# Optimization experiments

Measured on AMD Instinct MI355X. Metric: run time of the kernel, lower is better.

The kernel has to match this reference:

```python
import jax, jax.numpy as jnp
import numpy as np

N, D, G, C, M = 4096, 256, 4, 10, 5  # nodes, feat dim, batches, centroids, clusterings


def setup_inputs() -> dict:
    key = jax.random.key(0)
    k1, k2, k3, k4 = jax.random.split(key, 4)
    adj = jax.random.uniform(k1, (N, N), dtype=jnp.float32)
    enc_rep = jax.random.normal(k2, (N, D), dtype=jnp.float32)
    batch_id = jax.random.randint(k3, (N,), 0, G, dtype=jnp.int32)
    cluster_labels = jax.random.randint(k4, (M, N), 0, C, dtype=jnp.int32)
    return {"adj": adj, "enc_rep": enc_rep, "batch_id": batch_id,
            "cluster_labels": cluster_labels, "top_k": 20, "top_k_inter": 10}


def reference(adj, enc_rep, batch_id, cluster_labels, top_k, top_k_inter):
    n = enc_rep.shape[0]
    NEG = jnp.float32(-1e30)
    rows = jnp.arange(n)

    # 'similarity' metric: raw inner-product similarity, full N x N once
    sim = enc_rep @ enc_rep.T                                # [N, N]
    same = batch_id[:, None] == batch_id[None, :]            # same-batch mask

    # intra: top_k+1 within own batch group, drop first (self) column
    intra_sim = jnp.where(same, sim, NEG)
    _, intra_idx = jax.lax.top_k(intra_sim, top_k + 1)
    intra_idx = intra_idx[:, 1:]                              # [N, top_k]

    # inter: top_k_inter among all other batch groups
    inter_sim = jnp.where(same, NEG, sim)
    _, inter_idx = jax.lax.top_k(inter_sim, top_k_inter)      # [N, top_k_inter]

    knn_idx = jnp.concatenate([intra_idx, inter_idx], axis=1)  # [N, k_tot]

    # rep_adj[j, i] = 1 iff j is a knn of i  (coo rows=neighbors, cols=node)
    B = jnp.zeros((n, n), jnp.float32).at[knn_idx, rows[:, None]].set(1.0)
    # common_adj = rep_adj * (rep_adj.T > 0), diag zeroed (mutual-knn graph)
    common = B * B.T
    common = common.at[rows, rows].set(0.0)

    # locality = knn_neighbor * adj
    locality = common * adj

    # padded-neighbor validity mask (I_knn_padded != -1 analog): mutual neighbors
    mutual = common[rows[:, None], knn_idx] > 0               # [N, k_tot]

    # per-clustering close-neighbor test, combined across clusterings
    nb_lbl = cluster_labels[:, knn_idx]                       # [M, N, k_tot]
    eq = cluster_labels[:, :, None] == nb_lbl                 # [M, N, k_tot]
    curr = eq | mutual[None]                                  # curr_close_nei = eq | bool_mask
    all_close = jnp.all(curr, axis=0)                         # AND across clusterings

    return locality, all_close.astype(jnp.float32)
```

## Files before the change

kernel.cpp:

```cpp
#include <hip/hip_runtime.h>
#include <hip/hip_bf16.h>
#include <cfloat>

#define NN 4096
#define DD 256
#define MM 5
#define K_TOT 30
#define TGT_INTRA 32
#define TGT_INTER 24
#define CAND_CAP 64

typedef __attribute__((ext_vector_type(8))) short bf16x8;
typedef __attribute__((ext_vector_type(4))) float f32x4;

__device__ __forceinline__ void async16(const void* g, void* l) {
    __builtin_amdgcn_global_load_lds((__attribute__((address_space(1))) void*)g,
                                     (__attribute__((address_space(3))) void*)l,
                                     16, 0, 0);
}

__global__ __launch_bounds__(256) void convert_bf16(const float* __restrict__ E,
                                                    ushort* __restrict__ Eb) {
    const int idx = blockIdx.x * 256 + threadIdx.x;
    const float4 f = ((const float4*)E)[idx];
    ushort4 h;
    {
        __hip_bfloat16 a = __float2bfloat16(f.x); h.x = *(ushort*)&a;
        __hip_bfloat16 b = __float2bfloat16(f.y); h.y = *(ushort*)&b;
        __hip_bfloat16 c = __float2bfloat16(f.z); h.z = *(ushort*)&c;
        __hip_bfloat16 d = __float2bfloat16(f.w); h.w = *(ushort*)&d;
    }
    ((ushort4*)Eb)[idx] = h;
}

__global__ __launch_bounds__(256) void gemm_bf16(const ushort* __restrict__ Eb,
                                                 ushort* __restrict__ simb) {
    __shared__ union {
        struct { ushort A[128 * 32]; ushort B[128 * 32]; } s;
        ushort stage[128 * 136];
    } lds;

    const int t = threadIdx.x;
    const int w = t >> 6, lane = t & 63;
    const int quad = lane >> 4, mr = lane & 15;
    const int rowBase = blockIdx.y * 128, colBase = blockIdx.x * 128;
    const int waveRow = (w & 1) * 64, waveCol = (w >> 1) * 64;

    const int lrow = lane >> 2;
    const int lslot = lane & 3;
    const int gchunk = lslot ^ ((lrow >> 1) & 3);

    f32x4 acc[4][4];
#pragma unroll
    for (int a = 0; a < 4; ++a)
#pragma unroll
        for (int b = 0; b < 4; ++b) acc[a][b] = (f32x4)(0.0f);

    for (int kc = 0; kc < DD; kc += 32) {
#pragma unroll
        for (int n = 0; n < 2; ++n) {
            const int r = w * 32 + n * 16 + lrow;
            const ushort* ga = Eb + (size_t)(rowBase + r) * DD + kc + gchunk * 8;
            const ushort* gb = Eb + (size_t)(colBase + r) * DD + kc + gchunk * 8;
            async16(ga, &lds.s.A[(w * 32 + n * 16) * 32]);
            async16(gb, &lds.s.B[(w * 32 + n * 16) * 32]);
        }
        __syncthreads();

        const int swzF = (mr >> 1) & 3;
        bf16x8 af[4], bfr[4];
#pragma unroll
        for (int rt = 0; rt < 4; ++rt)
            af[rt] = *(const bf16x8*)&lds.s.A[(waveRow + rt * 16 + mr) * 32 +
                                              ((quad ^ swzF) * 8)];
#pragma unroll
        for (int ct = 0; ct < 4; ++ct)
            bfr[ct] = *(const bf16x8*)&lds.s.B[(waveCol + ct * 16 + mr) * 32 +
                                               ((quad ^ swzF) * 8)];
#pragma unroll
        for (int rt = 0; rt < 4; ++rt)
#pragma unroll
            for (int ct = 0; ct < 4; ++ct)
                acc[rt][ct] = __builtin_amdgcn_mfma_f32_16x16x32_bf16(
                    af[rt], bfr[ct], acc[rt][ct], 0, 0, 0);
        __syncthreads();
    }

#pragma unroll
    for (int rt = 0; rt < 4; ++rt)
#pragma unroll
        for (int ct = 0; ct < 4; ++ct)
#pragma unroll
            for (int reg = 0; reg < 4; ++reg) {
                __hip_bfloat16 hb = __float2bfloat16(acc[rt][ct][reg]);
                lds.stage[(waveRow + rt * 16 + quad * 4 + reg) * 136 +
                          waveCol + ct * 16 + mr] = *(ushort*)&hb;
            }
    __syncthreads();
#pragma unroll
    for (int it = 0; it < 8; ++it) {
        const int cid = t + it * 256;
        const int row = cid >> 4;
        const int off = (cid & 15) * 8;
        *(int4*)(simb + (size_t)(rowBase + row) * NN + colBase + off) =
            *(const int4*)&lds.stage[row * 136 + off];
    }
}

__global__ __launch_bounds__(256) void select_rescore(const ushort* __restrict__ sim,
                                                      const float* __restrict__ E,
                                                      const int* __restrict__ batch,
                                                      int* __restrict__ knn) {
    __shared__ unsigned hist[256];
    __shared__ unsigned subhist[256];
    __shared__ unsigned wsum[4];
    __shared__ int cb[2];
    __shared__ unsigned remc[2];
    __shared__ unsigned thrKey[2];
    __shared__ int candIdx[2][CAND_CAP];
    __shared__ double candVal[2][CAND_CAP];
    __shared__ int cnt[2];
    __shared__ float4 Ei4[DD / 4];

    const int i = blockIdx.x;
    const int t = threadIdx.x;
    const int lane = t & 63;
    const int w = t >> 6;
    const int bi = batch[i];

    hist[t] = 0u;
    subhist[t] = 0u;
    if (t < 128) ((int*)candIdx)[t] = 0x7FFFFFFF;
    if (t < 2) { cnt[t] = 0; cb[t] = 0; remc[t] = 1u; thrKey[t] = 0u; }
    if (t < DD / 4) Ei4[t] = ((const float4*)(E + (size_t)i * DD))[t];
    __syncthreads();

    unsigned short key[16];
    unsigned mmask = 0;
    {
        const ushort* sp = sim + (size_t)i * NN + t * 16;
        const int4 s0 = *(const int4*)sp;
        const int4 s1 = *(const int4*)(sp + 8);
        const unsigned sw[8] = {(unsigned)s0.x, (unsigned)s0.y, (unsigned)s0.z,
                                (unsigned)s0.w, (unsigned)s1.x, (unsigned)s1.y,
                                (unsigned)s1.z, (unsigned)s1.w};
        const int* bp = batch + t * 16;
        int bv[16];
        *(int4*)&bv[0] = *(const int4*)bp;
        *(int4*)&bv[4] = *(const int4*)(bp + 4);
        *(int4*)&bv[8] = *(const int4*)(bp + 8);
        *(int4*)&bv[12] = *(const int4*)(bp + 12);
#pragma unroll
        for (int c = 0; c < 16; ++c) {
            const unsigned u = (sw[c >> 1] >> ((c & 1) * 16)) & 0xFFFFu;
            const unsigned k = (u & 0x8000u) ? (u ^ 0xFFFFu) : (u | 0x8000u);
            key[c] = (unsigned short)k;
            const int m = (bv[c] == bi) ? 0 : 1;
            mmask |= (unsigned)m << c;
            atomicAdd(&hist[k >> 8], m ? 0x10000u : 1u);
        }
    }
    __syncthreads();

    {
        const int b = 255 - t;
        const unsigned h = hist[b];
        unsigned cum = h;
        for (int off = 1; off < 64; off <<= 1) {
            const unsigned o = __shfl_up(cum, off);
            if (lane >= off) cum += o;
        }
        if (lane == 63) wsum[w] = cum;
        __syncthreads();
        unsigned add = 0;
        for (int ww = 0; ww < w; ++ww) add += wsum[ww];
        cum += add;
        const unsigned cI = cum & 0xFFFFu, hI = h & 0xFFFFu;
        const unsigned cT = cum >> 16, hT = h >> 16;
        if (cI >= TGT_INTRA && cI - hI < TGT_INTRA) {
            cb[0] = b;
            remc[0] = TGT_INTRA - (cI - hI);
        }
        if (cT >= TGT_INTER && cT - hT < TGT_INTER) {
            cb[1] = b;
            remc[1] = TGT_INTER - (cT - hT);
        }
    }
    __syncthreads();

    {
        const int cb0 = cb[0], cb1 = cb[1];
#pragma unroll
        for (int c = 0; c < 16; ++c) {
            const int m = (mmask >> c) & 1;
            if ((int)(key[c] >> 8) == (m ? cb1 : cb0))
                atomicAdd(&subhist[key[c] & 0xFF], m ? 0x10000u : 1u);
        }
    }
    __syncthreads();

    {
        const unsigned rI = remc[0], rT = remc[1];
        const int cb0 = cb[0], cb1 = cb[1];
        const int b = 255 - t;
        const unsigned h = subhist[b];
        unsigned cum = h;
        for (int off = 1; off < 64; off <<= 1) {
            const unsigned o = __shfl_up(cum, off);
            if (lane >= off) cum += o;
        }
        if (lane == 63) wsum[w] = cum;
        __syncthreads();
        unsigned add = 0;
        for (int ww = 0; ww < w; ++ww) add += wsum[ww];
        cum += add;
        const unsigned cI = cum & 0xFFFFu, hI = h & 0xFFFFu;
        const unsigned cT = cum >> 16, hT = h >> 16;
        if (cI >= rI && cI - hI < rI) thrKey[0] = ((unsigned)cb0 << 8) | (unsigned)b;
        if (cT >= rT && cT - hT < rT) thrKey[1] = ((unsigned)cb1 << 8) | (unsigned)b;
    }
    __syncthreads();

    {
        const unsigned thr0 = thrKey[0], thr1 = thrKey[1];
#pragma unroll
        for (int c = 0; c < 16; ++c) {
            const int m = (mmask >> c) & 1;
            if ((unsigned)key[c] >= (m ? thr1 : thr0)) {
                const int pos = atomicAdd(&cnt[m], 1);
                if (pos < CAND_CAP) candIdx[m][pos] = t * 16 + c;
            }
        }
    }
    __syncthreads();

    if (t < 128) {
        const int m = t >> 6;
        const int slot = t & 63;
        const int c = min(cnt[m], CAND_CAP);
        double val = -DBL_MAX;
        if (slot < c) {
            const int j = candIdx[m][slot];
            const float* ej = E + (size_t)j * DD;
            const float* ei = (const float*)Ei4;
            double a0 = 0, a1 = 0, a2 = 0, a3 = 0;
#pragma unroll 8
            for (int k = 0; k < DD; k += 4) {
                const float4 e = *(const float4*)(ej + k);
                a0 = fma((double)ei[k + 0], (double)e.x, a0);
                a1 = fma((double)ei[k + 1], (double)e.y, a1);
                a2 = fma((double)ei[k + 2], (double)e.z, a2);
                a3 = fma((double)ei[k + 3], (double)e.w, a3);
            }
            val = (a0 + a1) + (a2 + a3);
        }
        candVal[m][slot] = val;
    }
    __syncthreads();

    if (w < 2) {
        const int m = w;
        double val = candVal[m][lane];
        int idx = candIdx[m][lane];
        const int rounds = (m == 0) ? 21 : 10;
        for (int q = 0; q < rounds; ++q) {
            double tv = val;
            int ti = idx;
#pragma unroll
            for (int off = 32; off; off >>= 1) {
                const double ov = __shfl_xor(tv, off);
                const int oi = __shfl_xor(ti, off);
                if (ov > tv || (ov == tv && oi < ti)) { tv = ov; ti = oi; }
            }
            if (lane == 0) {
                if (m == 0) { if (q > 0) knn[i * K_TOT + q - 1] = ti; }
                else        { knn[i * K_TOT + 20 + q] = ti; }
            }
            if (idx == ti) val = -DBL_MAX;
        }
    }
}

__global__ __launch_bounds__(256) void finalize_k(const int* __restrict__ knn,
                                                  const float* __restrict__ adj,
                                                  const int* __restrict__ cl,
                                                  float* __restrict__ out) {
    const int gid = blockIdx.x * 256 + threadIdx.x;
    if (gid >= NN * K_TOT) return;
    const int i = gid / K_TOT;
    const int j = knn[gid];

    bool mutual = false;
#pragma unroll
    for (int s = 0; s < K_TOT; ++s) mutual |= (knn[j * K_TOT + s] == i);

    if (mutual) out[(size_t)i * NN + j] = adj[(size_t)i * NN + j];

    bool ac = mutual;
    if (!ac) {
        bool alleq = true;
#pragma unroll
        for (int m = 0; m < MM; ++m) alleq &= (cl[m * NN + i] == cl[m * NN + j]);
        ac = alleq;
    }
    out[(size_t)NN * NN + gid] = ac ? 1.0f : 0.0f;
}

extern "C" void kernel_launch(void* const* d_in, const int* in_sizes, int n_in,
                              void* d_out, int out_size, void* d_ws, size_t ws_size,
                              hipStream_t stream) {
    const float* adj = (const float*)d_in[0];
    const float* enc = (const float*)d_in[1];
    const int* batch = (const int*)d_in[2];
    const int* cl = (const int*)d_in[3];
    float* out = (float*)d_out;

    const size_t simB = (size_t)NN * NN * sizeof(ushort);
    const size_t ebB = (size_t)NN * DD * sizeof(ushort);
    const size_t knnB = (size_t)NN * K_TOT * sizeof(int);

    const dim3 gGrid(NN / 128, NN / 128);

    if (ws_size >= simB + ebB + knnB) {
        ushort* simb = (ushort*)d_ws;
        ushort* Eb = (ushort*)((char*)d_ws + simB);
        int* knn = (int*)((char*)d_ws + simB + ebB);
        hipMemsetAsync(d_out, 0, (size_t)NN * NN * sizeof(float), stream);
        convert_bf16<<<NN * DD / 4 / 256, 256, 0, stream>>>(enc, Eb);
        gemm_bf16<<<gGrid, 256, 0, stream>>>(Eb, simb);
        select_rescore<<<NN, 256, 0, stream>>>(simb, enc, batch, knn);
        finalize_k<<<(NN * K_TOT + 255) / 256, 256, 0, stream>>>(knn, adj, cl, out);
    } else {
        ushort* simb = (ushort*)d_out;
        ushort* Eb = (ushort*)d_ws;
        int* knn = (int*)((char*)d_ws + ebB);
        convert_bf16<<<NN * DD / 4 / 256, 256, 0, stream>>>(enc, Eb);
        gemm_bf16<<<gGrid, 256, 0, stream>>>(Eb, simb);
        select_rescore<<<NN, 256, 0, stream>>>(simb, enc, batch, knn);
        hipMemsetAsync(d_out, 0, (size_t)NN * NN * sizeof(float), stream);
        finalize_k<<<(NN * K_TOT + 255) / 256, 256, 0, stream>>>(knn, adj, cl, out);
    }
}
```

Baseline: 227.2 us.

## Process one row per wavefront in top-k selection and shrink GEMM epilogue staging

The selection kernel now assigns one row per wavefront (four rows per block) rather than one row per 256-thread block. Each wave builds its radix histograms in its own shared-memory slice and scans them with wave shuffles instead of block-wide scans. The final top-k extraction now ranks each candidate by counting how many beat it, replacing repeated shuffle-argmax rounds. Separately, the GEMM epilogue stages output through LDS in four 32-row chunks to cut shared-memory use, which can raise occupancy but adds barriers.

```diff
diff --git a/kernel.cpp b/kernel.cpp
--- a/kernel.cpp
+++ b/kernel.cpp
@@ -37,7 +37,7 @@
                                                  ushort* __restrict__ simb) {
     __shared__ union {
         struct { ushort A[128 * 32]; ushort B[128 * 32]; } s;
-        ushort stage[128 * 136];
+        ushort stage[32 * 136];
     } lds;
 
     const int t = threadIdx.x;
@@ -87,23 +87,32 @@
     }
 
 #pragma unroll
-    for (int rt = 0; rt < 4; ++rt)
-#pragma unroll
-        for (int ct = 0; ct < 4; ++ct)
-#pragma unroll
-            for (int reg = 0; reg < 4; ++reg) {
-                __hip_bfloat16 hb = __float2bfloat16(acc[rt][ct][reg]);
-                lds.stage[(waveRow + rt * 16 + quad * 4 + reg) * 136 +
-                          waveCol + ct * 16 + mr] = *(ushort*)&hb;
-            }
-    __syncthreads();
-#pragma unroll
-    for (int it = 0; it < 8; ++it) {
-        const int cid = t + it * 256;
-        const int row = cid >> 4;
-        const int off = (cid & 15) * 8;
-        *(int4*)(simb + (size_t)(rowBase + row) * NN + colBase + off) =
-            *(const int4*)&lds.stage[row * 136 + off];
+    for (int c = 0; c < 4; ++c) {
+        __syncthreads();
+        if ((w & 1) == (c >> 1)) {
+            const int rtBase = 2 * (c & 1);
+#pragma unroll
+            for (int r2 = 0; r2 < 2; ++r2) {
+                const int rt = rtBase + r2;
+#pragma unroll
+                for (int ct = 0; ct < 4; ++ct)
+#pragma unroll
+                    for (int reg = 0; reg < 4; ++reg) {
+                        __hip_bfloat16 hb = __float2bfloat16(acc[rt][ct][reg]);
+                        const int lr2 = r2 * 16 + quad * 4 + reg;
+                        lds.stage[lr2 * 136 + waveCol + ct * 16 + mr] = *(ushort*)&hb;
+                    }
+            }
+        }
+        __syncthreads();
+#pragma unroll
+        for (int it = 0; it < 2; ++it) {
+            const int cid = t + it * 256;
+            const int row = cid >> 4;
+            const int off = (cid & 15) * 8;
+            *(int4*)(simb + (size_t)(rowBase + c * 32 + row) * NN + colBase + off) =
+                *(const int4*)&lds.stage[row * 136 + off];
+        }
     }
 }
 
@@ -111,173 +120,199 @@
                                                       const float* __restrict__ E,
                                                       const int* __restrict__ batch,
                                                       int* __restrict__ knn) {
-    __shared__ unsigned hist[256];
-    __shared__ unsigned subhist[256];
-    __shared__ unsigned wsum[4];
-    __shared__ int cb[2];
-    __shared__ unsigned remc[2];
-    __shared__ unsigned thrKey[2];
-    __shared__ int candIdx[2][CAND_CAP];
-    __shared__ double candVal[2][CAND_CAP];
-    __shared__ int cnt[2];
-    __shared__ float4 Ei4[DD / 4];
-
-    const int i = blockIdx.x;
+    __shared__ unsigned histS[4][256];
+    __shared__ unsigned subS[4][256];
+    __shared__ int candIdxS[4][2][CAND_CAP];
+    __shared__ double candValS[4][2][CAND_CAP];
+    __shared__ int cntS[4][2];
+    __shared__ int cbS[4][2];
+    __shared__ unsigned remS[4][2];
+    __shared__ unsigned thrS[4][2];
+
     const int t = threadIdx.x;
-    const int lane = t & 63;
-    const int w = t >> 6;
+    const int w = t >> 6, lane = t & 63;
+    const int i = __builtin_amdgcn_readfirstlane(blockIdx.x * 4 + w);
     const int bi = batch[i];
 
-    hist[t] = 0u;
-    subhist[t] = 0u;
-    if (t < 128) ((int*)candIdx)[t] = 0x7FFFFFFF;
-    if (t < 2) { cnt[t] = 0; cb[t] = 0; remc[t] = 1u; thrKey[t] = 0u; }
-    if (t < DD / 4) Ei4[t] = ((const float4*)(E + (size_t)i * DD))[t];
-    __syncthreads();
-
-    unsigned short key[16];
-    unsigned mmask = 0;
-    {
-        const ushort* sp = sim + (size_t)i * NN + t * 16;
-        const int4 s0 = *(const int4*)sp;
-        const int4 s1 = *(const int4*)(sp + 8);
-        const unsigned sw[8] = {(unsigned)s0.x, (unsigned)s0.y, (unsigned)s0.z,
-                                (unsigned)s0.w, (unsigned)s1.x, (unsigned)s1.y,
-                                (unsigned)s1.z, (unsigned)s1.w};
-        const int* bp = batch + t * 16;
-        int bv[16];
-        *(int4*)&bv[0] = *(const int4*)bp;
-        *(int4*)&bv[4] = *(const int4*)(bp + 4);
-        *(int4*)&bv[8] = *(const int4*)(bp + 8);
-        *(int4*)&bv[12] = *(const int4*)(bp + 12);
-#pragma unroll
-        for (int c = 0; c < 16; ++c) {
-            const unsigned u = (sw[c >> 1] >> ((c & 1) * 16)) & 0xFFFFu;
-            const unsigned k = (u & 0x8000u) ? (u ^ 0xFFFFu) : (u | 0x8000u);
-            key[c] = (unsigned short)k;
-            const int m = (bv[c] == bi) ? 0 : 1;
-            mmask |= (unsigned)m << c;
-            atomicAdd(&hist[k >> 8], m ? 0x10000u : 1u);
-        }
-    }
-    __syncthreads();
-
-    {
-        const int b = 255 - t;
-        const unsigned h = hist[b];
-        unsigned cum = h;
+    unsigned* hist = histS[w];
+    unsigned* sub = subS[w];
+
+#pragma unroll
+    for (int b = 0; b < 4; ++b) { hist[lane * 4 + b] = 0u; sub[lane * 4 + b] = 0u; }
+    if (lane < 2) cntS[w][lane] = 0;
+    __syncthreads();
+
+    unsigned kp[32];
+    unsigned long long interm = 0;
+    {
+        const ushort* sp = sim + (size_t)i * NN + lane * 8;
+        const int* bp = batch + lane * 8;
+#pragma unroll
+        for (int c = 0; c < 8; ++c) {
+            const int4 sv = *(const int4*)(sp + c * 512);
+            int bb[8];
+            *(int4*)&bb[0] = *(const int4*)(bp + c * 512);
+            *(int4*)&bb[4] = *(const int4*)(bp + c * 512 + 4);
+            const unsigned uu[4] = {(unsigned)sv.x, (unsigned)sv.y,
+                                    (unsigned)sv.z, (unsigned)sv.w};
+#pragma unroll
+            for (int p = 0; p < 4; ++p) {
+                const unsigned u = uu[p];
+                const unsigned sgn = u & 0x80008000u;
+                const unsigned k2 = u ^ (0x80008000u | ((sgn >> 15) * 0x7FFFu));
+                kp[c * 4 + p] = k2;
+                const int e0 = 2 * p, e1 = 2 * p + 1;
+                const unsigned m0 = (bb[e0] == bi) ? 0u : 1u;
+                const unsigned m1 = (bb[e1] == bi) ? 0u : 1u;
+                interm |= (unsigned long long)m0 << (c * 8 + e0);
+                interm |= (unsigned long long)m1 << (c * 8 + e1);
+                atomicAdd(&hist[(k2 >> 8) & 0xFF], m0 ? 0x10000u : 1u);
+                atomicAdd(&hist[k2 >> 24], m1 ? 0x10000u : 1u);
+            }
+        }
+    }
+    __syncthreads();
+
+    {
+        const unsigned* hb = &hist[lane * 4];
+        const unsigned s4 = hb[0] + hb[1] + hb[2] + hb[3];
+        unsigned suf = s4;
+#pragma unroll
         for (int off = 1; off < 64; off <<= 1) {
-            const unsigned o = __shfl_up(cum, off);
-            if (lane >= off) cum += o;
-        }
-        if (lane == 63) wsum[w] = cum;
-        __syncthreads();
-        unsigned add = 0;
-        for (int ww = 0; ww < w; ++ww) add += wsum[ww];
-        cum += add;
-        const unsigned cI = cum & 0xFFFFu, hI = h & 0xFFFFu;
-        const unsigned cT = cum >> 16, hT = h >> 16;
-        if (cI >= TGT_INTRA && cI - hI < TGT_INTRA) {
-            cb[0] = b;
-            remc[0] = TGT_INTRA - (cI - hI);
-        }
-        if (cT >= TGT_INTER && cT - hT < TGT_INTER) {
-            cb[1] = b;
-            remc[1] = TGT_INTER - (cT - hT);
-        }
-    }
-    __syncthreads();
-
-    {
-        const int cb0 = cb[0], cb1 = cb[1];
-#pragma unroll
-        for (int c = 0; c < 16; ++c) {
-            const int m = (mmask >> c) & 1;
-            if ((int)(key[c] >> 8) == (m ? cb1 : cb0))
-                atomicAdd(&subhist[key[c] & 0xFF], m ? 0x10000u : 1u);
-        }
-    }
-    __syncthreads();
-
-    {
-        const unsigned rI = remc[0], rT = remc[1];
-        const int cb0 = cb[0], cb1 = cb[1];
-        const int b = 255 - t;
-        const unsigned h = subhist[b];
-        unsigned cum = h;
+            const unsigned o = __shfl_down(suf, off);
+            if (lane + off < 64) suf += o;
+        }
+        unsigned cum = suf - s4;
+#pragma unroll
+        for (int b = 3; b >= 0; --b) {
+            const unsigned h = hb[b];
+            const unsigned prev = cum;
+            cum += h;
+            if ((cum & 0xFFFFu) >= TGT_INTRA && (prev & 0xFFFFu) < TGT_INTRA) {
+                cbS[w][0] = lane * 4 + b;
+                remS[w][0] = TGT_INTRA - (prev & 0xFFFFu);
+            }
+            if ((cum >> 16) >= TGT_INTER && (prev >> 16) < TGT_INTER) {
+                cbS[w][1] = lane * 4 + b;
+                remS[w][1] = TGT_INTER - (prev >> 16);
+            }
+        }
+    }
+    __syncthreads();
+
+    {
+        const int cb0 = cbS[w][0], cb1 = cbS[w][1];
+#pragma unroll
+        for (int c = 0; c < 8; ++c)
+#pragma unroll
+            for (int p = 0; p < 4; ++p) {
+                const unsigned k2 = kp[c * 4 + p];
+                const unsigned k0 = k2 & 0xFFFFu, k1 = k2 >> 16;
+                const int m0 = (interm >> (c * 8 + 2 * p)) & 1;
+                const int m1 = (interm >> (c * 8 + 2 * p + 1)) & 1;
+                if ((int)(k0 >> 8) == (m0 ? cb1 : cb0))
+                    atomicAdd(&sub[k0 & 0xFF], m0 ? 0x10000u : 1u);
+                if ((int)(k1 >> 8) == (m1 ? cb1 : cb0))
+                    atomicAdd(&sub[k1 & 0xFF], m1 ? 0x10000u : 1u);
+            }
+    }
+    __syncthreads();
+
+    {
+        const unsigned rI = remS[w][0], rT = remS[w][1];
+        const int cb0 = cbS[w][0], cb1 = cbS[w][1];
+        const unsigned* sb = &sub[lane * 4];
+        const unsigned s4 = sb[0] + sb[1] + sb[2] + sb[3];
+        unsigned suf = s4;
+#pragma unroll
         for (int off = 1; off < 64; off <<= 1) {
-            const unsigned o = __shfl_up(cum, off);
-            if (lane >= off) cum += o;
-        }
-        if (lane == 63) wsum[w] = cum;
-        __syncthreads();
-        unsigned add = 0;
-        for (int ww = 0; ww < w; ++ww) add += wsum[ww];
-        cum += add;
-        const unsigned cI = cum & 0xFFFFu, hI = h & 0xFFFFu;
-        const unsigned cT = cum >> 16, hT = h >> 16;
-        if (cI >= rI && cI - hI < rI) thrKey[0] = ((unsigned)cb0 << 8) | (unsigned)b;
-        if (cT >= rT && cT - hT < rT) thrKey[1] = ((unsigned)cb1 << 8) | (unsigned)b;
-    }
-    __syncthreads();
-
-    {
-        const unsigned thr0 = thrKey[0], thr1 = thrKey[1];
-#pragma unroll
-        for (int c = 0; c < 16; ++c) {
-            const int m = (mmask >> c) & 1;
-            if ((unsigned)key[c] >= (m ? thr1 : thr0)) {
-                const int pos = atomicAdd(&cnt[m], 1);
-                if (pos < CAND_CAP) candIdx[m][pos] = t * 16 + c;
-            }
-        }
-    }
-    __syncthreads();
-
-    if (t < 128) {
-        const int m = t >> 6;
-        const int slot = t & 63;
-        const int c = min(cnt[m], CAND_CAP);
-        double val = -DBL_MAX;
-        if (slot < c) {
-            const int j = candIdx[m][slot];
-            const float* ej = E + (size_t)j * DD;
-            const float* ei = (const float*)Ei4;
-            double a0 = 0, a1 = 0, a2 = 0, a3 = 0;
+            const unsigned o = __shfl_down(suf, off);
+            if (lane + off < 64) suf += o;
+        }
+        unsigned cum = suf - s4;
+#pragma unroll
+        for (int b = 3; b >= 0; --b) {
+            const unsigned h = sb[b];
+            const unsigned prev = cum;
+            cum += h;
+            if ((cum & 0xFFFFu) >= rI && (prev & 0xFFFFu) < rI)
+                thrS[w][0] = ((unsigned)cb0 << 8) | (unsigned)(lane * 4 + b);
+            if ((cum >> 16) >= rT && (prev >> 16) < rT)
+                thrS[w][1] = ((unsigned)cb1 << 8) | (unsigned)(lane * 4 + b);
+        }
+    }
+    __syncthreads();
+
+    {
+        const unsigned thr0 = thrS[w][0], thr1 = thrS[w][1];
+#pragma unroll
+        for (int c = 0; c < 8; ++c)
+#pragma unroll
+            for (int p = 0; p < 4; ++p) {
+                const unsigned k2 = kp[c * 4 + p];
+                const unsigned k0 = k2 & 0xFFFFu, k1 = k2 >> 16;
+                const int m0 = (interm >> (c * 8 + 2 * p)) & 1;
+                const int m1 = (interm >> (c * 8 + 2 * p + 1)) & 1;
+                if (k0 >= (m0 ? thr1 : thr0)) {
+                    const int pos = atomicAdd(&cntS[w][m0], 1);
+                    if (pos < CAND_CAP) candIdxS[w][m0][pos] = c * 512 + lane * 8 + 2 * p;
+                }
+                if (k1 >= (m1 ? thr1 : thr0)) {
+                    const int pos = atomicAdd(&cntS[w][m1], 1);
+                    if (pos < CAND_CAP) candIdxS[w][m1][pos] = c * 512 + lane * 8 + 2 * p + 1;
+                }
+            }
+    }
+    __syncthreads();
+
+    const int c0 = min(cntS[w][0], CAND_CAP);
+    const int c1 = min(cntS[w][1], CAND_CAP);
+    {
+        const int tot = c0 + c1;
+        const float* ei = E + (size_t)i * DD;
+        for (int base = 0; base < tot; base += 64) {
+            const int slot = base + lane;
+            if (slot < tot) {
+                const int m = (slot < c0) ? 0 : 1;
+                const int s = m ? (slot - c0) : slot;
+                const int j = candIdxS[w][m][s];
+                const float* ej = E + (size_t)j * DD;
+                double a0 = 0, a1 = 0, a2 = 0, a3 = 0;
 #pragma unroll 8
-            for (int k = 0; k < DD; k += 4) {
-                const float4 e = *(const float4*)(ej + k);
-                a0 = fma((double)ei[k + 0], (double)e.x, a0);
-                a1 = fma((double)ei[k + 1], (double)e.y, a1);
-                a2 = fma((double)ei[k + 2], (double)e.z, a2);
-                a3 = fma((double)ei[k + 3], (double)e.w, a3);
-            }
-            val = (a0 + a1) + (a2 + a3);
-        }
-        candVal[m][slot] = val;
-    }
-    __syncthreads();
-
-    if (w < 2) {
-        const int m = w;
-        double val = candVal[m][lane];
-        int idx = candIdx[m][lane];
-        const int rounds = (m == 0) ? 21 : 10;
-        for (int q = 0; q < rounds; ++q) {
-            double tv = val;
-            int ti = idx;
-#pragma unroll
-            for (int off = 32; off; off >>= 1) {
-                const double ov = __shfl_xor(tv, off);
-                const int oi = __shfl_xor(ti, off);
-                if (ov > tv || (ov == tv && oi < ti)) { tv = ov; ti = oi; }
-            }
-            if (lane == 0) {
-                if (m == 0) { if (q > 0) knn[i * K_TOT + q - 1] = ti; }
-                else        { knn[i * K_TOT + 20 + q] = ti; }
-            }
-            if (idx == ti) val = -DBL_MAX;
-        }
+                for (int k = 0; k < DD; k += 4) {
+                    const float4 e = *(const float4*)(ej + k);
+                    a0 = fma((double)ei[k + 0], (double)e.x, a0);
+                    a1 = fma((double)ei[k + 1], (double)e.y, a1);
+                    a2 = fma((double)ei[k + 2], (double)e.z, a2);
+                    a3 = fma((double)ei[k + 3], (double)e.w, a3);
+                }
+                candValS[w][m][s] = (a0 + a1) + (a2 + a3);
+            }
+        }
+    }
+    __syncthreads();
+
+    if (lane < c0) {
+        const double v = candValS[w][0][lane];
+        const int idx = candIdxS[w][0][lane];
+        int r = 0;
+        for (int s = 0; s < c0; ++s) {
+            const double o = candValS[w][0][s];
+            const int oi = candIdxS[w][0][s];
+            r += (o > v) || (o == v && oi < idx);
+        }
+        if (r >= 1 && r <= 20) knn[i * K_TOT + r - 1] = idx;
+    }
+    if (lane < c1) {
+        const double v = candValS[w][1][lane];
+        const int idx = candIdxS[w][1][lane];
+        int r = 0;
+        for (int s = 0; s < c1; ++s) {
+            const double o = candValS[w][1][s];
+            const int oi = candIdxS[w][1][s];
+            r += (o > v) || (o == v && oi < idx);
+        }
+        if (r < 10) knn[i * K_TOT + 20 + r] = idx;
     }
 }
 
@@ -328,7 +363,7 @@
         hipMemsetAsync(d_out, 0, (size_t)NN * NN * sizeof(float), stream);
         convert_bf16<<<NN * DD / 4 / 256, 256, 0, stream>>>(enc, Eb);
         gemm_bf16<<<gGrid, 256, 0, stream>>>(Eb, simb);
-        select_rescore<<<NN, 256, 0, stream>>>(simb, enc, batch, knn);
+        select_rescore<<<NN / 4, 256, 0, stream>>>(simb, enc, batch, knn);
         finalize_k<<<(NN * K_TOT + 255) / 256, 256, 0, stream>>>(knn, adj, cl, out);
     } else {
         ushort* simb = (ushort*)d_out;
@@ -336,7 +371,7 @@
         int* knn = (int*)((char*)d_ws + ebB);
         convert_bf16<<<NN * DD / 4 / 256, 256, 0, stream>>>(enc, Eb);
         gemm_bf16<<<gGrid, 256, 0, stream>>>(Eb, simb);
-        select_rescore<<<NN, 256, 0, stream>>>(simb, enc, batch, knn);
+        select_rescore<<<NN / 4, 256, 0, stream>>>(simb, enc, batch, knn);
         hipMemsetAsync(d_out, 0, (size_t)NN * NN * sizeof(float), stream);
         finalize_k<<<(NN * K_TOT + 255) / 256, 256, 0, stream>>>(knn, adj, cl, out);
     }
```

After: 212.9 us. 6.3% less time.
